# Kernel tuning notes

Hardware: AMD Instinct MI355X
Metric: run time of the kernel (lower is better)

## Reference

```python
import jax, jax.numpy as jnp
import numpy as np

N = 50000   # num_nodes
E = 800000  # num_edges (avg degree 16)
IN, H, OUT = 256, 128, 64
L = 4       # num_layers


def setup_inputs() -> dict:
    key = jax.random.key(0)
    ks = jax.random.split(key, 6)
    x = jax.random.normal(ks[0], (N, IN), jnp.float32)
    edge_index = jax.random.randint(ks[1], (2, E), 0, N, dtype=jnp.int64)
    W1 = jax.random.normal(ks[2], (IN, H), jnp.float32) / np.float32(np.sqrt(IN))
    b1 = jnp.zeros((H,), jnp.float32)
    Wr = jax.random.normal(ks[3], (L, H, H), jnp.float32) / np.float32(np.sqrt(H))
    eps = jnp.zeros((L,), jnp.float32)  # epsilons init to 0 as in the module
    W2 = jax.random.normal(ks[4], (H, OUT), jnp.float32) / np.float32(np.sqrt(H))
    b2 = jnp.zeros((OUT,), jnp.float32)
    return {"x": x, "W1": W1, "b1": b1, "Wr": Wr, "eps": eps,
            "W2": W2, "b2": b2, "edge_index": edge_index}


def reference(x, W1, b1, Wr, eps, W2, b2, edge_index):
    n = x.shape[0]
    # add self loops (done once in __init__ of the torch module)
    sl = jnp.arange(n, dtype=edge_index.dtype)
    row = jnp.concatenate([edge_index[0], sl])
    col = jnp.concatenate([edge_index[1], sl])
    # sym-normalized adjacency A_hat = D^-1/2 (A + I) D^-1/2; L_sym = I - A_hat
    deg = jax.ops.segment_sum(jnp.ones(row.shape, x.dtype), row, num_segments=n)
    dinv = jnp.where(deg > 0, jax.lax.rsqrt(deg), jnp.zeros_like(deg))
    w = dinv[row] * dinv[col]  # [E+N]

    def ahat(h):  # A_hat @ h via gather + segment scatter-add
        return jax.ops.segment_sum(w[:, None] * h[col], row, num_segments=n)

    h = jax.nn.relu(x @ W1 + b1)  # lin1 + ReLU (dropout = identity at eval)
    h0 = h
    for layer in range(Wr.shape[0]):
        h = h @ Wr[layer].T                 # lin_right (bias-free)
        h = 6.0 * h - 3.0 * ahat(h)         # 3 * (I + L_sym) @ h
        h0 = (1.0 + jnp.tanh(eps[layer])) * h0 + h  # epsilon-gated residual
        h = jax.nn.relu(h0)
    return h @ W2 + b2  # lin2 logits
```

## Files before the change

### kernel.cpp

```cpp
#include <hip/hip_runtime.h>
#include <math.h>


typedef __bf16 bf16x8 __attribute__((ext_vector_type(8)));
typedef float f32x4 __attribute__((ext_vector_type(4)));
typedef unsigned int uint32x4 __attribute__((ext_vector_type(4)));

__device__ __forceinline__ ushort f2bf(float f) {
  unsigned u = __float_as_uint(f);
  return (ushort)((u + 0x7fffu + ((u >> 16) & 1u)) >> 16);
}
__device__ __forceinline__ float bflo(unsigned u) { return __uint_as_float(u << 16); }
__device__ __forceinline__ float bfhi(unsigned u) { return __uint_as_float(u & 0xffff0000u); }

__global__ void k_count(const int* __restrict__ eidx, int* __restrict__ degi, int E, int n) {
  int e = blockIdx.x * blockDim.x + threadIdx.x;
  if (e < E) {
    int r = eidx[e];
    if ((unsigned)r < (unsigned)n) atomicAdd(&degi[r], 1);
  }
}

__global__ __launch_bounds__(1024) void k_scan1(const int* __restrict__ degi,
                                                int* __restrict__ rowstart,
                                                int* __restrict__ bsum, int n) {
  __shared__ int sm[1024];
  int tid = threadIdx.x;
  int i = blockIdx.x * 1024 + tid;
  int v = (i < n) ? degi[i] : 0;
  sm[tid] = v;
  __syncthreads();
  #pragma unroll
  for (int off = 1; off < 1024; off <<= 1) {
    int t = (tid >= off) ? sm[tid - off] : 0;
    __syncthreads();
    sm[tid] += t;
    __syncthreads();
  }
  if (i < n) rowstart[i] = sm[tid] - v;
  if (tid == 1023) bsum[blockIdx.x] = sm[1023];
}

__global__ void k_scan2(const int* __restrict__ bsum, int* __restrict__ boff, int nb) {
  if (threadIdx.x == 0 && blockIdx.x == 0) {
    int s = 0;
    for (int b = 0; b < nb; ++b) { boff[b] = s; s += bsum[b]; }
  }
}

__global__ __launch_bounds__(1024) void k_scan3(int* __restrict__ rowstart,
                                                const int* __restrict__ boff,
                                                int* __restrict__ cursor,
                                                const int* __restrict__ degi,
                                                float* __restrict__ dinv, int n, int E) {
  int i = blockIdx.x * 1024 + threadIdx.x;
  if (i < n) {
    int v = rowstart[i] + boff[blockIdx.x];
    rowstart[i] = v;
    cursor[i] = v;
    dinv[i] = rsqrtf((float)degi[i] + 1.0f);
  }
  if (i == 0) rowstart[n] = E;
}

template <typename IDX>
__global__ void k_fill(const int* __restrict__ eidx, int* __restrict__ cursor,
                       IDX* __restrict__ colidx, int E, int n) {
  int e = blockIdx.x * blockDim.x + threadIdx.x;
  if (e < E) {
    int r = eidx[e];
    int c = eidx[E + e];
    if ((unsigned)r < (unsigned)n && (unsigned)c < (unsigned)n) {
      int pos = atomicAdd(&cursor[r], 1);
      colidx[pos] = (IDX)c;
    }
  }
}

__global__ void k_cvt(const float* __restrict__ Wr, const float* __restrict__ W1,
                      const float* __restrict__ W2, ushort* __restrict__ wr_bf,
                      ushort* __restrict__ w1t, ushort* __restrict__ w2t,
                      int nwr, int nw1, int nw2) {
  int i = blockIdx.x * blockDim.x + threadIdx.x;
  if (i < nwr) {
    wr_bf[i] = f2bf(Wr[i]);
  } else if (i < nwr + nw1) {
    int m = i - nwr;
    int k = m >> 7, j = m & 127;
    w1t[j * 256 + k] = f2bf(W1[m]);
  } else if (i < nwr + nw1 + nw2) {
    int m = i - nwr - nw1;
    int k = m >> 6, j = m & 63;
    w2t[j * 128 + k] = f2bf(W2[m]);
  }
}

template <int K, int NOUT, bool AF32, int EPI>
__global__ __launch_bounds__(256) void mfma_gemm(const void* __restrict__ Ap,
                                                 const ushort* __restrict__ Bt,
                                                 const float* __restrict__ bias,
                                                 const float* __restrict__ dinv,
                                                 ushort* __restrict__ out_bf,
                                                 float* __restrict__ out_f32,
                                                 int n) {
  constexpr int KS = K / 32;
  constexpr int NT = NOUT / 16;
  const int lane = threadIdx.x & 63;
  const int wave = threadIdx.x >> 6;
  const int l15 = lane & 15;
  const int kq = lane >> 4;
  const int rowA = blockIdx.x * 64 + wave * 16 + l15;
  const bool arow_ok = rowA < n;

  f32x4 acc[NT];
  #pragma unroll
  for (int t = 0; t < NT; ++t) acc[t] = (f32x4){0.f, 0.f, 0.f, 0.f};

  #pragma unroll
  for (int kk = 0; kk < KS; ++kk) {
    bf16x8 a;
    if constexpr (AF32) {
      const float* A = (const float*)Ap;
      float4 f0 = make_float4(0.f, 0.f, 0.f, 0.f);
      float4 f1 = make_float4(0.f, 0.f, 0.f, 0.f);
      if (arow_ok) {
        f0 = *(const float4*)&A[(size_t)rowA * K + kk * 32 + kq * 8];
        f1 = *(const float4*)&A[(size_t)rowA * K + kk * 32 + kq * 8 + 4];
      }
      uint32x4 u;
      u[0] = (unsigned)f2bf(f0.x) | ((unsigned)f2bf(f0.y) << 16);
      u[1] = (unsigned)f2bf(f0.z) | ((unsigned)f2bf(f0.w) << 16);
      u[2] = (unsigned)f2bf(f1.x) | ((unsigned)f2bf(f1.y) << 16);
      u[3] = (unsigned)f2bf(f1.z) | ((unsigned)f2bf(f1.w) << 16);
      a = __builtin_bit_cast(bf16x8, u);
    } else {
      const ushort* A = (const ushort*)Ap;
      uint32x4 u = (uint32x4){0u, 0u, 0u, 0u};
      if (arow_ok) u = *(const uint32x4*)&A[(size_t)rowA * K + kk * 32 + kq * 8];
      a = __builtin_bit_cast(bf16x8, u);
    }
    #pragma unroll
    for (int t = 0; t < NT; ++t) {
      uint32x4 ub = *(const uint32x4*)&Bt[(size_t)(t * 16 + l15) * K + kk * 32 + kq * 8];
      bf16x8 b = __builtin_bit_cast(bf16x8, ub);
      acc[t] = __builtin_amdgcn_mfma_f32_16x16x32_bf16(a, b, acc[t], 0, 0, 0);
    }
  }

  const int rbase = blockIdx.x * 64 + wave * 16 + kq * 4;

  float bcol[NT];
  #pragma unroll
  for (int t = 0; t < NT; ++t) {
    if constexpr (EPI != 1) bcol[t] = bias[t * 16 + l15];
    else bcol[t] = 0.f;
  }
  float sc[4];
  #pragma unroll
  for (int r = 0; r < 4; ++r) {
    if constexpr (EPI == 1) sc[r] = (rbase + r < n) ? dinv[rbase + r] : 0.f;
    else sc[r] = 0.f;
  }

  #pragma unroll
  for (int r = 0; r < 4; ++r) {
    int row = rbase + r;
    if (row < n) {
      #pragma unroll
      for (int t = 0; t < NT; ++t) {
        int col = t * 16 + l15;
        float v = acc[t][r];
        if constexpr (EPI == 0) {
          v += bcol[t];
          v = fmaxf(v, 0.f);
          out_bf[(size_t)row * NOUT + col] = f2bf(v);
        } else if constexpr (EPI == 1) {
          out_bf[(size_t)row * NOUT + col] = f2bf(v * sc[r]);
        } else {
          out_f32[(size_t)row * NOUT + col] = v + bcol[t];
        }
      }
    }
  }
}

template <typename IDX>
__global__ __launch_bounds__(256) void k_spmm3(const ushort* __restrict__ pre,
                                               const float* __restrict__ dinv,
                                               const int* __restrict__ rowstart,
                                               const IDX* __restrict__ colidx,
                                               const float* __restrict__ eps, int layer,
                                               const ushort* __restrict__ h0in,
                                               ushort* __restrict__ h0out,
                                               ushort* __restrict__ hbf, int n) {
  const int lane = threadIdx.x & 63;
  const int r = blockIdx.x * 4 + (threadIdx.x >> 6);
  if (r >= n) return;

  const int s0 = rowstart[r], s1 = rowstart[r + 1];
  const float dr = dinv[r];
  const int half = lane >> 5;
  const int c4 = lane & 31;
  const size_t rowb = (size_t)r * 128 + c4 * 4;

  const uint2 pr = *(const uint2*)&pre[rowb];
  const uint2 h0u = *(const uint2*)&h0in[rowb];

  float a0 = 0.f, a1 = 0.f, a2 = 0.f, a3 = 0.f;
  for (int base = s0; base < s1; base += 64) {
    int m = s1 - base; if (m > 64) m = 64;
    int ci = 0;
    if (base + lane < s1) ci = (int)colidx[base + lane];
    int full = m >> 1;
    int i = 0;
    for (; i + 3 < full; i += 4) {
      int cA = __shfl(ci, 2 * i + half);
      int cB = __shfl(ci, 2 * i + 2 + half);
      int cC = __shfl(ci, 2 * i + 4 + half);
      int cD = __shfl(ci, 2 * i + 6 + half);
      uint2 uA = *(const uint2*)&pre[(size_t)cA * 128 + c4 * 4];
      uint2 uB = *(const uint2*)&pre[(size_t)cB * 128 + c4 * 4];
      uint2 uC = *(const uint2*)&pre[(size_t)cC * 128 + c4 * 4];
      uint2 uD = *(const uint2*)&pre[(size_t)cD * 128 + c4 * 4];
      a0 += bflo(uA.x); a1 += bfhi(uA.x); a2 += bflo(uA.y); a3 += bfhi(uA.y);
      a0 += bflo(uB.x); a1 += bfhi(uB.x); a2 += bflo(uB.y); a3 += bfhi(uB.y);
      a0 += bflo(uC.x); a1 += bfhi(uC.x); a2 += bflo(uC.y); a3 += bfhi(uC.y);
      a0 += bflo(uD.x); a1 += bfhi(uD.x); a2 += bflo(uD.y); a3 += bfhi(uD.y);
    }
    for (; i < full; ++i) {
      int cA = __shfl(ci, 2 * i + half);
      uint2 uA = *(const uint2*)&pre[(size_t)cA * 128 + c4 * 4];
      a0 += bflo(uA.x); a1 += bfhi(uA.x); a2 += bflo(uA.y); a3 += bfhi(uA.y);
    }
    if (m & 1) {
      int cZ = __shfl(ci, m - 1);
      if (half == 0) {
        uint2 uZ = *(const uint2*)&pre[(size_t)cZ * 128 + c4 * 4];
        a0 += bflo(uZ.x); a1 += bfhi(uZ.x); a2 += bflo(uZ.y); a3 += bfhi(uZ.y);
      }
    }
  }
  a0 += __shfl_xor(a0, 32);
  a1 += __shfl_xor(a1, 32);
  a2 += __shfl_xor(a2, 32);
  a3 += __shfl_xor(a3, 32);

  if (half == 0) {
    const float aa = (6.0f - 3.0f * dr * dr) / dr;
    const float m3 = -3.0f * dr;
    const float g = 1.0f + tanhf(eps[layer]);
    float v0 = g * bflo(h0u.x) + aa * bflo(pr.x) + m3 * a0;
    float v1 = g * bfhi(h0u.x) + aa * bfhi(pr.x) + m3 * a1;
    float v2 = g * bflo(h0u.y) + aa * bflo(pr.y) + m3 * a2;
    float v3 = g * bfhi(h0u.y) + aa * bfhi(pr.y) + m3 * a3;
    uint2 ho, hr;
    ho.x = (unsigned)f2bf(v0) | ((unsigned)f2bf(v1) << 16);
    ho.y = (unsigned)f2bf(v2) | ((unsigned)f2bf(v3) << 16);
    hr.x = (unsigned)f2bf(fmaxf(v0, 0.f)) | ((unsigned)f2bf(fmaxf(v1, 0.f)) << 16);
    hr.y = (unsigned)f2bf(fmaxf(v2, 0.f)) | ((unsigned)f2bf(fmaxf(v3, 0.f)) << 16);
    *(uint2*)&h0out[rowb] = ho;
    *(uint2*)&hbf[rowb] = hr;
  }
}

extern "C" void kernel_launch(void* const* d_in, const int* in_sizes, int n_in,
                              void* d_out, int out_size, void* d_ws, size_t ws_size,
                              hipStream_t stream) {
  const float* x   = (const float*)d_in[0];
  const float* W1  = (const float*)d_in[1];
  const float* b1  = (const float*)d_in[2];
  const float* Wr  = (const float*)d_in[3];
  const float* eps = (const float*)d_in[4];
  const float* W2  = (const float*)d_in[5];
  const float* b2  = (const float*)d_in[6];
  const int*   eidx= (const int*)d_in[7];

  const int IN = 256, H = 128, OUT = 64;
  const int n = in_sizes[0] / IN;
  const int E = in_sizes[7] / 2;
  const int L = in_sizes[4];

  size_t off = 0;
  auto carve = [&](size_t bytes) -> void* {
    void* p = (char*)d_ws + off;
    off += (bytes + 255) & ~(size_t)255;
    return p;
  };
  int*    degi     = (int*)carve((size_t)n * 4);
  int*    rowstart = (int*)carve((size_t)(n + 1) * 4);
  int*    cursor   = (int*)carve((size_t)n * 4);
  int*    bsum     = (int*)carve(64 * 4);
  int*    boff     = (int*)carve(64 * 4);
  void*   colidx   = carve((size_t)E * 4);
  float*  dinv     = (float*)carve((size_t)n * 4);
  ushort* h0bf     = (ushort*)carve((size_t)n * H * 2);
  ushort* hbf      = (ushort*)carve((size_t)n * H * 2);
  ushort* pre      = (ushort*)carve((size_t)n * H * 2);
  ushort* wr_bf    = (ushort*)carve((size_t)L * H * H * 2);
  ushort* w1t      = (ushort*)carve((size_t)IN * H * 2);
  ushort* w2t      = (ushort*)carve((size_t)H * OUT * 2);
  if (off > ws_size) return;

  const bool small = (n < 65536);

  hipMemsetAsync(degi, 0, (size_t)n * 4, stream);
  k_count<<<(E + 255) / 256, 256, 0, stream>>>(eidx, degi, E, n);
  int nwr = L * H * H, nw1 = IN * H, nw2 = H * OUT;
  k_cvt<<<(nwr + nw1 + nw2 + 255) / 256, 256, 0, stream>>>(Wr, W1, W2, wr_bf, w1t, w2t,
                                                           nwr, nw1, nw2);
  int nb = (n + 1023) / 1024;
  k_scan1<<<nb, 1024, 0, stream>>>(degi, rowstart, bsum, n);
  k_scan2<<<1, 64, 0, stream>>>(bsum, boff, nb);
  k_scan3<<<nb, 1024, 0, stream>>>(rowstart, boff, cursor, degi, dinv, n, E);
  if (small)
    k_fill<ushort><<<(E + 255) / 256, 256, 0, stream>>>(eidx, cursor, (ushort*)colidx, E, n);
  else
    k_fill<int><<<(E + 255) / 256, 256, 0, stream>>>(eidx, cursor, (int*)colidx, E, n);

  int gx = (n + 63) / 64;
  mfma_gemm<256, 128, true, 0><<<gx, 256, 0, stream>>>(x, w1t, b1, nullptr, hbf, nullptr, n);
  for (int l = 0; l < L; ++l) {
    mfma_gemm<128, 128, false, 1><<<gx, 256, 0, stream>>>(
        hbf, wr_bf + (size_t)l * H * H, nullptr, dinv, pre, nullptr, n);
    const ushort* h0in = (l == 0) ? hbf : h0bf;
    if (small)
      k_spmm3<ushort><<<(n + 3) / 4, 256, 0, stream>>>(pre, dinv, rowstart,
          (const ushort*)colidx, eps, l, h0in, h0bf, hbf, n);
    else
      k_spmm3<int><<<(n + 3) / 4, 256, 0, stream>>>(pre, dinv, rowstart,
          (const int*)colidx, eps, l, h0in, h0bf, hbf, n);
  }
  mfma_gemm<128, 64, false, 2><<<gx, 256, 0, stream>>>(hbf, w2t, b2, nullptr, nullptr,
                                                       (float*)d_out, n);
}
```

Measured before the change: 465.0 us.

## Split GEMM columns across waves and widen SpMM gathers to 16-byte loads

The GEMM kernel now divides output columns between pairs of waves (CW=2), so each block covers 32 rows and each wave holds half as many accumulators. The grid doubles to improve occupancy and load balance. The SpMM kernel has each group of 16 lanes load a full 128-column row with 16-byte vector loads, so four neighbour rows are gathered at once instead of two. The cost is an extra cross-lane reduction stage, a harder tail when the edge count is not a multiple of four, and A-tile reads duplicated across the wave pairs in the GEMM.

After: 463.3 us. No clear change (-0.4%).

```diff
diff --git a/kernel.cpp b/kernel.cpp
--- a/kernel.cpp
+++ b/kernel.cpp
@@ -95,7 +95,7 @@
   }
 }
 
-template <int K, int NOUT, bool AF32, int EPI>
+template <int K, int NOUT, int CW, bool AF32, int EPI>
 __global__ __launch_bounds__(256) void mfma_gemm(const void* __restrict__ Ap,
                                                  const ushort* __restrict__ Bt,
                                                  const float* __restrict__ bias,
@@ -104,12 +104,16 @@
                                                  float* __restrict__ out_f32,
                                                  int n) {
   constexpr int KS = K / 32;
-  constexpr int NT = NOUT / 16;
+  constexpr int NT = NOUT / 16 / CW;
+  constexpr int ROWS = (4 / CW) * 16;
   const int lane = threadIdx.x & 63;
   const int wave = threadIdx.x >> 6;
+  const int rw = wave / CW;
+  const int cw = wave % CW;
   const int l15 = lane & 15;
   const int kq = lane >> 4;
-  const int rowA = blockIdx.x * 64 + wave * 16 + l15;
+  const int col0 = cw * (NOUT / CW);
+  const int rowA = blockIdx.x * ROWS + rw * 16 + l15;
   const bool arow_ok = rowA < n;
 
   f32x4 acc[NT];
@@ -141,18 +145,18 @@
     }
     #pragma unroll
     for (int t = 0; t < NT; ++t) {
-      uint32x4 ub = *(const uint32x4*)&Bt[(size_t)(t * 16 + l15) * K + kk * 32 + kq * 8];
+      uint32x4 ub = *(const uint32x4*)&Bt[(size_t)(col0 + t * 16 + l15) * K + kk * 32 + kq * 8];
       bf16x8 b = __builtin_bit_cast(bf16x8, ub);
       acc[t] = __builtin_amdgcn_mfma_f32_16x16x32_bf16(a, b, acc[t], 0, 0, 0);
     }
   }
 
-  const int rbase = blockIdx.x * 64 + wave * 16 + kq * 4;
+  const int rbase = blockIdx.x * ROWS + rw * 16 + kq * 4;
 
   float bcol[NT];
   #pragma unroll
   for (int t = 0; t < NT; ++t) {
-    if constexpr (EPI != 1) bcol[t] = bias[t * 16 + l15];
+    if constexpr (EPI != 1) bcol[t] = bias[col0 + t * 16 + l15];
     else bcol[t] = 0.f;
   }
   float sc[4];
@@ -168,7 +172,7 @@
     if (row < n) {
       #pragma unroll
       for (int t = 0; t < NT; ++t) {
-        int col = t * 16 + l15;
+        int col = col0 + t * 16 + l15;
         float v = acc[t][r];
         if constexpr (EPI == 0) {
           v += bcol[t];
@@ -185,7 +189,7 @@
 }
 
 template <typename IDX>
-__global__ __launch_bounds__(256) void k_spmm3(const ushort* __restrict__ pre,
+__global__ __launch_bounds__(256) void k_spmm4(const ushort* __restrict__ pre,
                                                const float* __restrict__ dinv,
                                                const int* __restrict__ rowstart,
                                                const IDX* __restrict__ colidx,
@@ -199,67 +203,88 @@
 
   const int s0 = rowstart[r], s1 = rowstart[r + 1];
   const float dr = dinv[r];
-  const int half = lane >> 5;
-  const int c4 = lane & 31;
-  const size_t rowb = (size_t)r * 128 + c4 * 4;
-
-  const uint2 pr = *(const uint2*)&pre[rowb];
-  const uint2 h0u = *(const uint2*)&h0in[rowb];
+  const int q = lane >> 4;
+  const int c8 = lane & 15;
+  const size_t rowb = (size_t)r * 128 + c8 * 8;
+
+  const uint32x4 pr = *(const uint32x4*)&pre[rowb];
+  const uint32x4 h0u = *(const uint32x4*)&h0in[rowb];
 
   float a0 = 0.f, a1 = 0.f, a2 = 0.f, a3 = 0.f;
+  float a4 = 0.f, a5 = 0.f, a6 = 0.f, a7 = 0.f;
+
   for (int base = s0; base < s1; base += 64) {
     int m = s1 - base; if (m > 64) m = 64;
     int ci = 0;
     if (base + lane < s1) ci = (int)colidx[base + lane];
-    int full = m >> 1;
+    int full4 = m >> 2;
     int i = 0;
-    for (; i + 3 < full; i += 4) {
-      int cA = __shfl(ci, 2 * i + half);
-      int cB = __shfl(ci, 2 * i + 2 + half);
-      int cC = __shfl(ci, 2 * i + 4 + half);
-      int cD = __shfl(ci, 2 * i + 6 + half);
-      uint2 uA = *(const uint2*)&pre[(size_t)cA * 128 + c4 * 4];
-      uint2 uB = *(const uint2*)&pre[(size_t)cB * 128 + c4 * 4];
-      uint2 uC = *(const uint2*)&pre[(size_t)cC * 128 + c4 * 4];
-      uint2 uD = *(const uint2*)&pre[(size_t)cD * 128 + c4 * 4];
-      a0 += bflo(uA.x); a1 += bfhi(uA.x); a2 += bflo(uA.y); a3 += bfhi(uA.y);
-      a0 += bflo(uB.x); a1 += bfhi(uB.x); a2 += bflo(uB.y); a3 += bfhi(uB.y);
-      a0 += bflo(uC.x); a1 += bfhi(uC.x); a2 += bflo(uC.y); a3 += bfhi(uC.y);
-      a0 += bflo(uD.x); a1 += bfhi(uD.x); a2 += bflo(uD.y); a3 += bfhi(uD.y);
-    }
-    for (; i < full; ++i) {
-      int cA = __shfl(ci, 2 * i + half);
-      uint2 uA = *(const uint2*)&pre[(size_t)cA * 128 + c4 * 4];
-      a0 += bflo(uA.x); a1 += bfhi(uA.x); a2 += bflo(uA.y); a3 += bfhi(uA.y);
-    }
-    if (m & 1) {
-      int cZ = __shfl(ci, m - 1);
-      if (half == 0) {
-        uint2 uZ = *(const uint2*)&pre[(size_t)cZ * 128 + c4 * 4];
-        a0 += bflo(uZ.x); a1 += bfhi(uZ.x); a2 += bflo(uZ.y); a3 += bfhi(uZ.y);
+    for (; i + 3 < full4; i += 4) {
+      int cA = __shfl(ci, 4 * i + q);
+      int cB = __shfl(ci, 4 * i + 4 + q);
+      int cC = __shfl(ci, 4 * i + 8 + q);
+      int cD = __shfl(ci, 4 * i + 12 + q);
+      uint32x4 uA = *(const uint32x4*)&pre[(size_t)cA * 128 + c8 * 8];
+      uint32x4 uB = *(const uint32x4*)&pre[(size_t)cB * 128 + c8 * 8];
+      uint32x4 uC = *(const uint32x4*)&pre[(size_t)cC * 128 + c8 * 8];
+      uint32x4 uD = *(const uint32x4*)&pre[(size_t)cD * 128 + c8 * 8];
+      a0 += bflo(uA[0]); a1 += bfhi(uA[0]); a2 += bflo(uA[1]); a3 += bfhi(uA[1]);
+      a4 += bflo(uA[2]); a5 += bfhi(uA[2]); a6 += bflo(uA[3]); a7 += bfhi(uA[3]);
+      a0 += bflo(uB[0]); a1 += bfhi(uB[0]); a2 += bflo(uB[1]); a3 += bfhi(uB[1]);
+      a4 += bflo(uB[2]); a5 += bfhi(uB[2]); a6 += bflo(uB[3]); a7 += bfhi(uB[3]);
+      a0 += bflo(uC[0]); a1 += bfhi(uC[0]); a2 += bflo(uC[1]); a3 += bfhi(uC[1]);
+      a4 += bflo(uC[2]); a5 += bfhi(uC[2]); a6 += bflo(uC[3]); a7 += bfhi(uC[3]);
+      a0 += bflo(uD[0]); a1 += bfhi(uD[0]); a2 += bflo(uD[1]); a3 += bfhi(uD[1]);
+      a4 += bflo(uD[2]); a5 += bfhi(uD[2]); a6 += bflo(uD[3]); a7 += bfhi(uD[3]);
+    }
+    for (; i < full4; ++i) {
+      int cA = __shfl(ci, 4 * i + q);
+      uint32x4 uA = *(const uint32x4*)&pre[(size_t)cA * 128 + c8 * 8];
+      a0 += bflo(uA[0]); a1 += bfhi(uA[0]); a2 += bflo(uA[1]); a3 += bfhi(uA[1]);
+      a4 += bflo(uA[2]); a5 += bfhi(uA[2]); a6 += bflo(uA[3]); a7 += bfhi(uA[3]);
+    }
+    int rem = m & 3;
+    if (rem) {
+      int cZ = __shfl(ci, full4 * 4 + (q < rem ? q : 0));
+      if (q < rem) {
+        uint32x4 uZ = *(const uint32x4*)&pre[(size_t)cZ * 128 + c8 * 8];
+        a0 += bflo(uZ[0]); a1 += bfhi(uZ[0]); a2 += bflo(uZ[1]); a3 += bfhi(uZ[1]);
+        a4 += bflo(uZ[2]); a5 += bfhi(uZ[2]); a6 += bflo(uZ[3]); a7 += bfhi(uZ[3]);
       }
     }
   }
-  a0 += __shfl_xor(a0, 32);
-  a1 += __shfl_xor(a1, 32);
-  a2 += __shfl_xor(a2, 32);
-  a3 += __shfl_xor(a3, 32);
-
-  if (half == 0) {
+  a0 += __shfl_xor(a0, 16); a1 += __shfl_xor(a1, 16);
+  a2 += __shfl_xor(a2, 16); a3 += __shfl_xor(a3, 16);
+  a4 += __shfl_xor(a4, 16); a5 += __shfl_xor(a5, 16);
+  a6 += __shfl_xor(a6, 16); a7 += __shfl_xor(a7, 16);
+  a0 += __shfl_xor(a0, 32); a1 += __shfl_xor(a1, 32);
+  a2 += __shfl_xor(a2, 32); a3 += __shfl_xor(a3, 32);
+  a4 += __shfl_xor(a4, 32); a5 += __shfl_xor(a5, 32);
+  a6 += __shfl_xor(a6, 32); a7 += __shfl_xor(a7, 32);
+
+  if (q == 0) {
     const float aa = (6.0f - 3.0f * dr * dr) / dr;
     const float m3 = -3.0f * dr;
     const float g = 1.0f + tanhf(eps[layer]);
-    float v0 = g * bflo(h0u.x) + aa * bflo(pr.x) + m3 * a0;
-    float v1 = g * bfhi(h0u.x) + aa * bfhi(pr.x) + m3 * a1;
-    float v2 = g * bflo(h0u.y) + aa * bflo(pr.y) + m3 * a2;
-    float v3 = g * bfhi(h0u.y) + aa * bfhi(pr.y) + m3 * a3;
-    uint2 ho, hr;
-    ho.x = (unsigned)f2bf(v0) | ((unsigned)f2bf(v1) << 16);
-    ho.y = (unsigned)f2bf(v2) | ((unsigned)f2bf(v3) << 16);
-    hr.x = (unsigned)f2bf(fmaxf(v0, 0.f)) | ((unsigned)f2bf(fmaxf(v1, 0.f)) << 16);
-    hr.y = (unsigned)f2bf(fmaxf(v2, 0.f)) | ((unsigned)f2bf(fmaxf(v3, 0.f)) << 16);
-    *(uint2*)&h0out[rowb] = ho;
-    *(uint2*)&hbf[rowb] = hr;
+    float v0 = g * bflo(h0u[0]) + aa * bflo(pr[0]) + m3 * a0;
+    float v1 = g * bfhi(h0u[0]) + aa * bfhi(pr[0]) + m3 * a1;
+    float v2 = g * bflo(h0u[1]) + aa * bflo(pr[1]) + m3 * a2;
+    float v3 = g * bfhi(h0u[1]) + aa * bfhi(pr[1]) + m3 * a3;
+    float v4 = g * bflo(h0u[2]) + aa * bflo(pr[2]) + m3 * a4;
+    float v5 = g * bfhi(h0u[2]) + aa * bfhi(pr[2]) + m3 * a5;
+    float v6 = g * bflo(h0u[3]) + aa * bflo(pr[3]) + m3 * a6;
+    float v7 = g * bfhi(h0u[3]) + aa * bfhi(pr[3]) + m3 * a7;
+    uint32x4 ho, hr;
+    ho[0] = (unsigned)f2bf(v0) | ((unsigned)f2bf(v1) << 16);
+    ho[1] = (unsigned)f2bf(v2) | ((unsigned)f2bf(v3) << 16);
+    ho[2] = (unsigned)f2bf(v4) | ((unsigned)f2bf(v5) << 16);
+    ho[3] = (unsigned)f2bf(v6) | ((unsigned)f2bf(v7) << 16);
+    hr[0] = (unsigned)f2bf(fmaxf(v0, 0.f)) | ((unsigned)f2bf(fmaxf(v1, 0.f)) << 16);
+    hr[1] = (unsigned)f2bf(fmaxf(v2, 0.f)) | ((unsigned)f2bf(fmaxf(v3, 0.f)) << 16);
+    hr[2] = (unsigned)f2bf(fmaxf(v4, 0.f)) | ((unsigned)f2bf(fmaxf(v5, 0.f)) << 16);
+    hr[3] = (unsigned)f2bf(fmaxf(v6, 0.f)) | ((unsigned)f2bf(fmaxf(v7, 0.f)) << 16);
+    *(uint32x4*)&h0out[rowb] = ho;
+    *(uint32x4*)&hbf[rowb] = hr;
   }
 }
 
@@ -317,19 +342,20 @@
   else
     k_fill<int><<<(E + 255) / 256, 256, 0, stream>>>(eidx, cursor, (int*)colidx, E, n);
 
-  int gx = (n + 63) / 64;
-  mfma_gemm<256, 128, true, 0><<<gx, 256, 0, stream>>>(x, w1t, b1, nullptr, hbf, nullptr, n);
+  int gx32 = (n + 31) / 32;
+  mfma_gemm<256, 128, 2, true, 0><<<gx32, 256, 0, stream>>>(x, w1t, b1, nullptr, hbf,
+                                                            nullptr, n);
   for (int l = 0; l < L; ++l) {
-    mfma_gemm<128, 128, false, 1><<<gx, 256, 0, stream>>>(
+    mfma_gemm<128, 128, 2, false, 1><<<gx32, 256, 0, stream>>>(
         hbf, wr_bf + (size_t)l * H * H, nullptr, dinv, pre, nullptr, n);
     const ushort* h0in = (l == 0) ? hbf : h0bf;
     if (small)
-      k_spmm3<ushort><<<(n + 3) / 4, 256, 0, stream>>>(pre, dinv, rowstart,
+      k_spmm4<ushort><<<(n + 3) / 4, 256, 0, stream>>>(pre, dinv, rowstart,
           (const ushort*)colidx, eps, l, h0in, h0bf, hbf, n);
     else
-      k_spmm3<int><<<(n + 3) / 4, 256, 0, stream>>>(pre, dinv, rowstart,
+      k_spmm4<int><<<(n + 3) / 4, 256, 0, stream>>>(pre, dinv, rowstart,
           (const int*)colidx, eps, l, h0in, h0bf, hbf, n);
   }
-  mfma_gemm<128, 64, false, 2><<<gx, 256, 0, stream>>>(hbf, w2t, b2, nullptr, nullptr,
-                                                       (float*)d_out, n);
-}
+  mfma_gemm<128, 64, 2, false, 2><<<gx32, 256, 0, stream>>>(hbf, w2t, b2, nullptr, nullptr,
+                                                            (float*)d_out, n);
+}
```

## Split SpMM into column-slab passes and restructure GEMM with column-split waves

Applied to the files above, without the earlier changes.

The SpMM now runs four passes, each gathering one 32-column slab of the neighbor features with 8 lanes per edge and 8 edges in flight per wave. The aim is a smaller working set per pass that fits in cache and more concurrent gathers. The GEMM splits each block's output columns across wave pairs (32 rows per block) and loads all A and B fragments for a K-half into registers before the MFMAs, to expose more memory-level parallelism. The cost is rowstart/colidx reads repeated four times per SpMM row, more shuffle reductions, and twice as many GEMM blocks.

After: 623.2 us. 34.0% more time.

```diff
diff --git a/kernel.cpp b/kernel.cpp
--- a/kernel.cpp
+++ b/kernel.cpp
@@ -95,7 +95,7 @@
   }
 }
 
-template <int K, int NOUT, bool AF32, int EPI>
+template <int K, int NOUT, int CW, bool AF32, int EPI>
 __global__ __launch_bounds__(256) void mfma_gemm(const void* __restrict__ Ap,
                                                  const ushort* __restrict__ Bt,
                                                  const float* __restrict__ bias,
@@ -103,13 +103,18 @@
                                                  ushort* __restrict__ out_bf,
                                                  float* __restrict__ out_f32,
                                                  int n) {
-  constexpr int KS = K / 32;
-  constexpr int NT = NOUT / 16;
+  constexpr int KH = (K > 128) ? 2 : 1;
+  constexpr int KSH = K / 32 / KH;
+  constexpr int NT = NOUT / 16 / CW;
+  constexpr int ROWS = (4 / CW) * 16;
   const int lane = threadIdx.x & 63;
   const int wave = threadIdx.x >> 6;
+  const int rw = wave / CW;
+  const int cw = wave % CW;
   const int l15 = lane & 15;
   const int kq = lane >> 4;
-  const int rowA = blockIdx.x * 64 + wave * 16 + l15;
+  const int col0 = cw * (NOUT / CW);
+  const int rowA = blockIdx.x * ROWS + rw * 16 + l15;
   const bool arow_ok = rowA < n;
 
   f32x4 acc[NT];
@@ -117,42 +122,79 @@
   for (int t = 0; t < NT; ++t) acc[t] = (f32x4){0.f, 0.f, 0.f, 0.f};
 
   #pragma unroll
-  for (int kk = 0; kk < KS; ++kk) {
-    bf16x8 a;
+  for (int h = 0; h < KH; ++h) {
+    const int kbase = h * 128;
+    uint32x4 areg[KSH];
     if constexpr (AF32) {
       const float* A = (const float*)Ap;
-      float4 f0 = make_float4(0.f, 0.f, 0.f, 0.f);
-      float4 f1 = make_float4(0.f, 0.f, 0.f, 0.f);
-      if (arow_ok) {
-        f0 = *(const float4*)&A[(size_t)rowA * K + kk * 32 + kq * 8];
-        f1 = *(const float4*)&A[(size_t)rowA * K + kk * 32 + kq * 8 + 4];
-      }
-      uint32x4 u;
-      u[0] = (unsigned)f2bf(f0.x) | ((unsigned)f2bf(f0.y) << 16);
-      u[1] = (unsigned)f2bf(f0.z) | ((unsigned)f2bf(f0.w) << 16);
-      u[2] = (unsigned)f2bf(f1.x) | ((unsigned)f2bf(f1.y) << 16);
-      u[3] = (unsigned)f2bf(f1.z) | ((unsigned)f2bf(f1.w) << 16);
-      a = __builtin_bit_cast(bf16x8, u);
+      float4 f0[KSH], f1[KSH];
+      #pragma unroll
+      for (int kk = 0; kk < KSH; ++kk) {
+        f0[kk] = make_float4(0.f, 0.f, 0.f, 0.f);
+        f1[kk] = make_float4(0.f, 0.f, 0.f, 0.f);
+        if (arow_ok) {
+          f0[kk] = *(const float4*)&A[(size_t)rowA * K + kbase + kk * 32 + kq * 8];
+          f1[kk] = *(const float4*)&A[(size_t)rowA * K + kbase + kk * 32 + kq * 8 + 4];
+        }
+      }
+      uint32x4 breg[KSH][NT];
+      #pragma unroll
+      for (int kk = 0; kk < KSH; ++kk)
+        #pragma unroll
+        for (int t = 0; t < NT; ++t)
+          breg[kk][t] = *(const uint32x4*)&Bt[(size_t)(col0 + t * 16 + l15) * K +
+                                              kbase + kk * 32 + kq * 8];
+      #pragma unroll
+      for (int kk = 0; kk < KSH; ++kk) {
+        uint32x4 u;
+        u[0] = (unsigned)f2bf(f0[kk].x) | ((unsigned)f2bf(f0[kk].y) << 16);
+        u[1] = (unsigned)f2bf(f0[kk].z) | ((unsigned)f2bf(f0[kk].w) << 16);
+        u[2] = (unsigned)f2bf(f1[kk].x) | ((unsigned)f2bf(f1[kk].y) << 16);
+        u[3] = (unsigned)f2bf(f1[kk].z) | ((unsigned)f2bf(f1[kk].w) << 16);
+        areg[kk] = u;
+      }
+      #pragma unroll
+      for (int kk = 0; kk < KSH; ++kk) {
+        bf16x8 a = __builtin_bit_cast(bf16x8, areg[kk]);
+        #pragma unroll
+        for (int t = 0; t < NT; ++t) {
+          bf16x8 b = __builtin_bit_cast(bf16x8, breg[kk][t]);
+          acc[t] = __builtin_amdgcn_mfma_f32_16x16x32_bf16(a, b, acc[t], 0, 0, 0);
+        }
+      }
     } else {
       const ushort* A = (const ushort*)Ap;
-      uint32x4 u = (uint32x4){0u, 0u, 0u, 0u};
-      if (arow_ok) u = *(const uint32x4*)&A[(size_t)rowA * K + kk * 32 + kq * 8];
-      a = __builtin_bit_cast(bf16x8, u);
-    }
-    #pragma unroll
-    for (int t = 0; t < NT; ++t) {
-      uint32x4 ub = *(const uint32x4*)&Bt[(size_t)(t * 16 + l15) * K + kk * 32 + kq * 8];
-      bf16x8 b = __builtin_bit_cast(bf16x8, ub);
-      acc[t] = __builtin_amdgcn_mfma_f32_16x16x32_bf16(a, b, acc[t], 0, 0, 0);
-    }
-  }
-
-  const int rbase = blockIdx.x * 64 + wave * 16 + kq * 4;
+      #pragma unroll
+      for (int kk = 0; kk < KSH; ++kk) {
+        areg[kk] = (uint32x4){0u, 0u, 0u, 0u};
+        if (arow_ok)
+          areg[kk] = *(const uint32x4*)&A[(size_t)rowA * K + kbase + kk * 32 + kq * 8];
+      }
+      uint32x4 breg[KSH][NT];
+      #pragma unroll
+      for (int kk = 0; kk < KSH; ++kk)
+        #pragma unroll
+        for (int t = 0; t < NT; ++t)
+          breg[kk][t] = *(const uint32x4*)&Bt[(size_t)(col0 + t * 16 + l15) * K +
+                                              kbase + kk * 32 + kq * 8];
+      #pragma unroll
+      for (int kk = 0; kk < KSH; ++kk) {
+        bf16x8 a = __builtin_bit_cast(bf16x8, areg[kk]);
+        #pragma unroll
+        for (int t = 0; t < NT; ++t) {
+          bf16x8 b = __builtin_bit_cast(bf16x8, breg[kk][t]);
+          acc[t] = __builtin_amdgcn_mfma_f32_16x16x32_bf16(a, b, acc[t], 0, 0, 0);
+        }
+      }
+    }
+  }
+
+  const int rbase = blockIdx.x * ROWS + rw * 16 + kq * 4;
 
   float bcol[NT];
   #pragma unroll
   for (int t = 0; t < NT; ++t) {
-    if constexpr (EPI != 1) bcol[t] = bias[t * 16 + l15];
+    if constexpr (EPI != 1) bcol[t] = bias[col0 + t * 16 + l15];
     else bcol[t] = 0.f;
   }
   float sc[4];
@@ -168,7 +210,7 @@
     if (row < n) {
       #pragma unroll
       for (int t = 0; t < NT; ++t) {
-        int col = t * 16 + l15;
+        int col = col0 + t * 16 + l15;
         float v = acc[t][r];
         if constexpr (EPI == 0) {
           v += bcol[t];
@@ -185,7 +227,7 @@
 }
 
 template <typename IDX>
-__global__ __launch_bounds__(256) void k_spmm3(const ushort* __restrict__ pre,
+__global__ __launch_bounds__(256) void k_spmm5(const ushort* __restrict__ pre,
                                                const float* __restrict__ dinv,
                                                const int* __restrict__ rowstart,
                                                const IDX* __restrict__ colidx,
@@ -193,59 +235,61 @@
                                                const ushort* __restrict__ h0in,
                                                ushort* __restrict__ h0out,
                                                ushort* __restrict__ hbf, int n) {
+  const int nb4 = gridDim.x >> 2;
+  const int pass = blockIdx.x / nb4;
+  const int bid = blockIdx.x - pass * nb4;
   const int lane = threadIdx.x & 63;
-  const int r = blockIdx.x * 4 + (threadIdx.x >> 6);
+  const int r = bid * 4 + (threadIdx.x >> 6);
   if (r >= n) return;
 
   const int s0 = rowstart[r], s1 = rowstart[r + 1];
   const float dr = dinv[r];
-  const int half = lane >> 5;
-  const int c4 = lane & 31;
-  const size_t rowb = (size_t)r * 128 + c4 * 4;
+  const int oct = lane >> 3;
+  const int c8 = lane & 7;
+  const int slab = pass * 32;
+  const size_t rowb = (size_t)r * 128 + slab + c8 * 4;
 
   const uint2 pr = *(const uint2*)&pre[rowb];
   const uint2 h0u = *(const uint2*)&h0in[rowb];
 
   float a0 = 0.f, a1 = 0.f, a2 = 0.f, a3 = 0.f;
+
   for (int base = s0; base < s1; base += 64) {
     int m = s1 - base; if (m > 64) m = 64;
     int ci = 0;
     if (base + lane < s1) ci = (int)colidx[base + lane];
-    int full = m >> 1;
+    int full8 = m >> 3;
     int i = 0;
-    for (; i + 3 < full; i += 4) {
-      int cA = __shfl(ci, 2 * i + half);
-      int cB = __shfl(ci, 2 * i + 2 + half);
-      int cC = __shfl(ci, 2 * i + 4 + half);
-      int cD = __shfl(ci, 2 * i + 6 + half);
-      uint2 uA = *(const uint2*)&pre[(size_t)cA * 128 + c4 * 4];
-      uint2 uB = *(const uint2*)&pre[(size_t)cB * 128 + c4 * 4];
-      uint2 uC = *(const uint2*)&pre[(size_t)cC * 128 + c4 * 4];
-      uint2 uD = *(const uint2*)&pre[(size_t)cD * 128 + c4 * 4];
+    for (; i + 1 < full8; i += 2) {
+      int cA = __shfl(ci, 8 * i + oct);
+      int cB = __shfl(ci, 8 * i + 8 + oct);
+      uint2 uA = *(const uint2*)&pre[(size_t)cA * 128 + slab + c8 * 4];
+      uint2 uB = *(const uint2*)&pre[(size_t)cB * 128 + slab + c8 * 4];
       a0 += bflo(uA.x); a1 += bfhi(uA.x); a2 += bflo(uA.y); a3 += bfhi(uA.y);
       a0 += bflo(uB.x); a1 += bfhi(uB.x); a2 += bflo(uB.y); a3 += bfhi(uB.y);
-      a0 += bflo(uC.x); a1 += bfhi(uC.x); a2 += bflo(uC.y); a3 += bfhi(uC.y);
-      a0 += bflo(uD.x); a1 += bfhi(uD.x); a2 += bflo(uD.y); a3 += bfhi(uD.y);
-    }
-    for (; i < full; ++i) {
-      int cA = __shfl(ci, 2 * i + half);
-      uint2 uA = *(const uint2*)&pre[(size_t)cA * 128 + c4 * 4];
+    }
+    for (; i < full8; ++i) {
+      int cA = __shfl(ci, 8 * i + oct);
+      uint2 uA = *(const uint2*)&pre[(size_t)cA * 128 + slab + c8 * 4];
       a0 += bflo(uA.x); a1 += bfhi(uA.x); a2 += bflo(uA.y); a3 += bfhi(uA.y);
     }
-    if (m & 1) {
-      int cZ = __shfl(ci, m - 1);
-      if (half == 0) {
-        uint2 uZ = *(const uint2*)&pre[(size_t)cZ * 128 + c4 * 4];
+    int rem = m & 7;
+    if (rem) {
+      int cZ = __shfl(ci, full8 * 8 + (oct < rem ? oct : 0));
+      if (oct < rem) {
+        uint2 uZ = *(const uint2*)&pre[(size_t)cZ * 128 + slab + c8 * 4];
         a0 += bflo(uZ.x); a1 += bfhi(uZ.x); a2 += bflo(uZ.y); a3 += bfhi(uZ.y);
       }
     }
   }
-  a0 += __shfl_xor(a0, 32);
-  a1 += __shfl_xor(a1, 32);
-  a2 += __shfl_xor(a2, 32);
-  a3 += __shfl_xor(a3, 32);
-
-  if (half == 0) {
+  a0 += __shfl_xor(a0, 8);  a1 += __shfl_xor(a1, 8);
+  a2 += __shfl_xor(a2, 8);  a3 += __shfl_xor(a3, 8);
+  a0 += __shfl_xor(a0, 16); a1 += __shfl_xor(a1, 16);
+  a2 += __shfl_xor(a2, 16); a3 += __shfl_xor(a3, 16);
+  a0 += __shfl_xor(a0, 32); a1 += __shfl_xor(a1, 32);
+  a2 += __shfl_xor(a2, 32); a3 += __shfl_xor(a3, 32);
+
+  if (oct == 0) {
     const float aa = (6.0f - 3.0f * dr * dr) / dr;
     const float m3 = -3.0f * dr;
     const float g = 1.0f + tanhf(eps[layer]);
@@ -317,19 +361,21 @@
   else
     k_fill<int><<<(E + 255) / 256, 256, 0, stream>>>(eidx, cursor, (int*)colidx, E, n);
 
-  int gx = (n + 63) / 64;
-  mfma_gemm<256, 128, true, 0><<<gx, 256, 0, stream>>>(x, w1t, b1, nullptr, hbf, nullptr, n);
+  int gx32 = (n + 31) / 32;
+  int nb4 = (n + 3) / 4;
+  mfma_gemm<256, 128, 2, true, 0><<<gx32, 256, 0, stream>>>(x, w1t, b1, nullptr, hbf,
+                                                            nullptr, n);
   for (int l = 0; l < L; ++l) {
-    mfma_gemm<128, 128, false, 1><<<gx, 256, 0, stream>>>(
+    mfma_gemm<128, 128, 2, false, 1><<<gx32, 256, 0, stream>>>(
         hbf, wr_bf + (size_t)l * H * H, nullptr, dinv, pre, nullptr, n);
     const ushort* h0in = (l == 0) ? hbf : h0bf;
     if (small)
-      k_spmm3<ushort><<<(n + 3) / 4, 256, 0, stream>>>(pre, dinv, rowstart,
+      k_spmm5<ushort><<<4 * nb4, 256, 0, stream>>>(pre, dinv, rowstart,
           (const ushort*)colidx, eps, l, h0in, h0bf, hbf, n);
     else
-      k_spmm3<int><<<(n + 3) / 4, 256, 0, stream>>>(pre, dinv, rowstart,
+      k_spmm5<int><<<4 * nb4, 256, 0, stream>>>(pre, dinv, rowstart,
           (const int*)colidx, eps, l, h0in, h0bf, hbf, n);
   }
-  mfma_gemm<128, 64, false, 2><<<gx, 256, 0, stream>>>(hbf, w2t, b2, nullptr, nullptr,
-                                                       (float*)d_out, n);
-}
+  mfma_gemm<128, 64, 2, false, 2><<<gx32, 256, 0, stream>>>(hbf, w2t, b2, nullptr, nullptr,
+                                                            (float*)d_out, n);
+}
```
